# Kernel tuning notes

Hardware: AMD Instinct MI355X
Metric: run time of the kernel (lower is better)

The kernel has to match this reference:

```python
import jax, jax.numpy as jnp
import numpy as np

B, C, E, S, L, N = 2, 256, 256, 3, 5, 128
HMAX = 128
LEVEL_SIZES = np.array([128, 64, 32, 16, 8])
STRIDES = np.array([8.0, 16.0, 32.0, 64.0, 128.0])
GROUPS = 8
EPS = 1e-5


def setup_inputs() -> dict:
    key = jax.random.key(0)
    ks = jax.random.split(key, 16)
    # Padded FPN pyramid stacked as [L, B, C, HMAX, HMAX]; level l valid in [:sz, :sz]
    fm = jnp.zeros((L, B, C, HMAX, HMAX), jnp.float32)
    for l in range(L):
        sz = int(LEVEL_SIZES[l])
        fm = fm.at[l, :, :, :sz, :sz].set(jax.random.normal(ks[l], (B, C, sz, sz), jnp.float32))
    # Boxes in 1024x1024 image coordinates (x1, y1, x2, y2)
    cxy = jax.random.uniform(ks[5], (N, 2), minval=60.0, maxval=960.0)
    wh = jax.random.uniform(ks[6], (N, 2), minval=8.0, maxval=96.0)
    boxes = jnp.concatenate([cxy - wh / 2, cxy + wh / 2], axis=1)
    batch_idx = jax.random.randint(ks[7], (N,), 0, B, jnp.int32)
    level_idx = jax.random.randint(ks[8], (N,), 0, L, jnp.int32)
    sym_ids = jax.random.randint(ks[9], (N,), 0, 6, jnp.int32)
    conv_w = jax.random.normal(ks[10], (E, C, 3, 3), jnp.float32) / np.float32(np.sqrt(C * 9))
    gn_scale = jnp.ones((E,), jnp.float32)
    gn_bias = jnp.zeros((E,), jnp.float32)
    head_w = jax.random.normal(ks[11], (E, E), jnp.float32) / np.float32(np.sqrt(E))
    head_b = jnp.zeros((E,), jnp.float32)
    spat_w = jax.random.normal(ks[12], (E, 4), jnp.float32) * 0.01
    spat_b = jnp.zeros((E,), jnp.float32)
    sym_emb = jax.random.normal(ks[13], (6, E), jnp.float32) * 0.05
    fuse_w = jax.random.normal(ks[14], (6, E, E), jnp.float32) / np.float32(np.sqrt(E))
    fuse_b = jnp.zeros((6, E), jnp.float32)
    return dict(feature_maps=fm, boxes=boxes, conv_w=conv_w, gn_scale=gn_scale,
                gn_bias=gn_bias, head_w=head_w, head_b=head_b, spat_w=spat_w,
                spat_b=spat_b, sym_emb=sym_emb, fuse_w=fuse_w, fuse_b=fuse_b,
                batch_idx=batch_idx, level_idx=level_idx, sym_ids=sym_ids)


def _roi_align(fm, boxes, batch_idx, level_idx):
    # Batched roi_align (aligned=False, sampling_ratio=1) over all boxes at once.
    scale = (1.0 / jnp.asarray(STRIDES, fm.dtype))[level_idx]          # [N]
    hv = jnp.asarray(LEVEL_SIZES, fm.dtype)[level_idx]                 # [N] valid H=W per box
    x1 = boxes[:, 0] * scale; y1 = boxes[:, 1] * scale
    x2 = boxes[:, 2] * scale; y2 = boxes[:, 3] * scale
    roi_w = jnp.maximum(x2 - x1, 1.0)
    roi_h = jnp.maximum(y2 - y1, 1.0)
    off = (jnp.arange(S, dtype=fm.dtype) + 0.5) / S                    # bin centers
    xs = x1[:, None] + off[None, :] * roi_w[:, None]                   # [N,S]
    ys = y1[:, None] + off[None, :] * roi_h[:, None]                   # [N,S]
    y = jnp.broadcast_to(ys[:, :, None], (ys.shape[0], S, S))          # [N,S,S]
    x = jnp.broadcast_to(xs[:, None, :], (xs.shape[0], S, S))
    hvb = hv[:, None, None]
    valid = (y > -1.0) & (y < hvb) & (x > -1.0) & (x < hvb)
    yc = jnp.clip(y, 0.0, hvb - 1.0)
    xc = jnp.clip(x, 0.0, hvb - 1.0)
    y0 = jnp.floor(yc).astype(jnp.int32)
    x0 = jnp.floor(xc).astype(jnp.int32)
    hi = (hvb - 1.0).astype(jnp.int32)
    y1i = jnp.minimum(y0 + 1, hi)
    x1i = jnp.minimum(x0 + 1, hi)
    ly = yc - y0.astype(fm.dtype)
    lx = xc - x0.astype(fm.dtype)
    lvl = level_idx[:, None, None]
    bix = batch_idx[:, None, None]

    def g(yi, xi):
        # gather only the 4 corner pixels -> [N,S,S,C]
        return fm[lvl, bix, :, yi, xi]

    v = ((1 - ly) * (1 - lx))[..., None] * g(y0, x0) \
      + ((1 - ly) * lx)[..., None] * g(y0, x1i) \
      + (ly * (1 - lx))[..., None] * g(y1i, x0) \
      + (ly * lx)[..., None] * g(y1i, x1i)
    v = jnp.where(valid[..., None], v, 0.0)
    return jnp.transpose(v, (0, 3, 1, 2))                              # [N,C,S,S]


def _forward(feature_maps, boxes, conv_w, gn_scale, gn_bias, head_w, head_b,
             spat_w, spat_b, sym_emb, fuse_w, fuse_b, batch_idx, level_idx, sym_ids):
    roi = _roi_align(feature_maps, boxes, batch_idx, level_idx)        # [N,C,S,S]
    h = jax.lax.conv_general_dilated(roi, conv_w, (1, 1), ((1, 1), (1, 1)),
                                     dimension_numbers=('NCHW', 'OIHW', 'NCHW'))  # [N,E,S,S]
    n = h.shape[0]
    hg = h.reshape(n, GROUPS, -1)
    mu = hg.mean(-1, keepdims=True)
    var = hg.var(-1, keepdims=True)
    hg = (hg - mu) * jax.lax.rsqrt(var + EPS)
    h = hg.reshape(h.shape) * gn_scale[None, :, None, None] + gn_bias[None, :, None, None]
    h = jax.nn.relu(h)
    h = h.reshape(n, E, -1).mean(-1)                                   # spatial mean -> [N,E]
    head_out = jax.nn.relu(h @ head_w.T + head_b)                      # sym_feat_nn + ReLU
    spat = jax.nn.relu(boxes @ spat_w.T + spat_b)                      # spatial_embeddings
    fused_in = head_out + spat + sym_emb[sym_ids]                      # + class embedding
    out = jax.nn.relu(jnp.einsum('ne,nfe->nf', fused_in, fuse_w[sym_ids]) + fuse_b[sym_ids])
    return out                                                          # [N,E]


def reference(feature_maps, boxes, conv_w, gn_scale, gn_bias, head_w, head_b,
              spat_w, spat_b, sym_emb, fuse_w, fuse_b, batch_idx, level_idx, sym_ids):
    return _forward(feature_maps, boxes, conv_w, gn_scale, gn_bias, head_w, head_b,
                    spat_w, spat_b, sym_emb, fuse_w, fuse_b, batch_idx, level_idx, sym_ids)
```

## Files before the change

### kernel.cpp

```cpp
#include <hip/hip_runtime.h>
#include <hip/hip_bf16.h>


__device__ __forceinline__ float bf_lo(unsigned u) { return __uint_as_float(u << 16); }
__device__ __forceinline__ float bf_hi(unsigned u) { return __uint_as_float(u & 0xffff0000u); }
__device__ __forceinline__ unsigned short f2bf(float f) {
    __hip_bfloat16 h = __float2bfloat16(f);
    return *(unsigned short*)&h;
}

__global__ __launch_bounds__(256) void prep_k(
    const float* __restrict__ conv_w,
    const float* __restrict__ head_w, const float* __restrict__ fuse_w,
    const float* __restrict__ fm, const float* __restrict__ boxes,
    const int* __restrict__ batch_idx, const int* __restrict__ level_idx,
    unsigned short* __restrict__ w8, unsigned short* __restrict__ w9,
    float* __restrict__ head_wT, float* __restrict__ fuse_wT,
    float* __restrict__ roiT) {
    int blk = blockIdx.x;
    int t = threadIdx.x;

    if (blk < 256) {
        int c = blk, e = t;
        const float* src = conv_w + ((size_t)e * 256 + c) * 9;
        unsigned short tmp[8];
#pragma unroll
        for (int k = 0; k < 8; ++k) tmp[k] = f2bf(src[k]);
        ((uint4*)w8)[(size_t)c * 256 + e] = *(const uint4*)tmp;
        w9[(size_t)c * 256 + e] = f2bf(src[8]);
        return;
    }

    if (blk < 704) {
        __shared__ float tile[32][33];
        int q = blk - 256;
        int z = q >> 6;
        int rem = q & 63;
        int bx = (rem & 7) * 32, by = (rem >> 3) * 32;
        const float* in = (z == 0) ? head_w : fuse_w + (size_t)(z - 1) * 65536;
        float* out = (z == 0) ? head_wT : fuse_wT + (size_t)(z - 1) * 65536;
        int tx = t & 31, ty = t >> 5;
#pragma unroll
        for (int i = 0; i < 32; i += 8)
            tile[ty + i][tx] = in[(size_t)(by + ty + i) * 256 + bx + tx];
        __syncthreads();
#pragma unroll
        for (int i = 0; i < 32; i += 8)
            out[(size_t)(bx + ty + i) * 256 + by + tx] = tile[tx][ty + i];
        return;
    }

    {
        int q = blk - 704;
        int n = q / 9, p = q % 9;
        int i = p / 3, j = p % 3;
        int c = t;

        int lvl = level_idx[n];
        int b = batch_idx[n];
        const float sizes[5]  = {128.f, 64.f, 32.f, 16.f, 8.f};
        const float invstr[5] = {1.f/8.f, 1.f/16.f, 1.f/32.f, 1.f/64.f, 1.f/128.f};
        float scale = invstr[lvl];
        float hv = sizes[lvl];

        float x1 = boxes[n*4+0] * scale, y1 = boxes[n*4+1] * scale;
        float x2 = boxes[n*4+2] * scale, y2 = boxes[n*4+3] * scale;
        float rw = fmaxf(x2 - x1, 1.f), rh = fmaxf(y2 - y1, 1.f);
        float x = x1 + (((float)j + 0.5f) / 3.f) * rw;
        float y = y1 + (((float)i + 0.5f) / 3.f) * rh;

        bool valid = (y > -1.f) && (y < hv) && (x > -1.f) && (x < hv);
        float yc = fminf(fmaxf(y, 0.f), hv - 1.f);
        float xc = fminf(fmaxf(x, 0.f), hv - 1.f);
        int y0 = (int)floorf(yc), x0 = (int)floorf(xc);
        int hi = (int)(hv - 1.f);
        int y1i = min(y0 + 1, hi), x1i = min(x0 + 1, hi);
        float ly = yc - (float)y0, lx = xc - (float)x0;

        const float* base = fm + (((size_t)lvl * 2 + b) * 256 + c) * (128 * 128);
        float v00 = base[y0 * 128 + x0];
        float v01 = base[y0 * 128 + x1i];
        float v10 = base[y1i * 128 + x0];
        float v11 = base[y1i * 128 + x1i];
        float v = (1.f - ly) * (1.f - lx) * v00 + (1.f - ly) * lx * v01 +
                  ly * (1.f - lx) * v10 + ly * lx * v11;
        roiT[((size_t)n * 9 + p) * 256 + c] = valid ? v : 0.f;
    }
}

__global__ __launch_bounds__(512, 2) void conv_gn_pool(
    const float* __restrict__ roiT,
    const unsigned short* __restrict__ w8, const unsigned short* __restrict__ w9,
    const float* __restrict__ gn_scale, const float* __restrict__ gn_bias,
    float* __restrict__ pooled) {
    __shared__ float lds_roi[256 * 12];
    __shared__ float red[4 * 64 * 9];

    int n  = blockIdx.x >> 2;
    int eq = blockIdx.x & 3;
    int t = threadIdx.x;
    int e_loc = t & 63;
    int ch = t >> 6;
    int e = eq * 64 + e_loc;

    const float4* rsrc4 = (const float4*)(roiT + (size_t)n * 2304);
    for (int v4 = t; v4 < 576; v4 += 512) {
        float4 rv = rsrc4[v4];
        int p = v4 / 64, c4 = (v4 & 63) * 4;
        lds_roi[(c4 + 0) * 12 + p] = rv.x;
        lds_roi[(c4 + 1) * 12 + p] = rv.y;
        lds_roi[(c4 + 2) * 12 + p] = rv.z;
        lds_roi[(c4 + 3) * 12 + p] = rv.w;
    }
    __syncthreads();

    float accx[9], accy[9];
#pragma unroll
    for (int p = 0; p < 9; ++p) { accx[p] = 0.f; accy[p] = 0.f; }

    int c0 = ch * 32;
    for (int c = c0; c < c0 + 32; c += 2) {
        float ra[9], rb[9];
#pragma unroll
        for (int jj = 0; jj < 9; ++jj) {
            ra[jj] = lds_roi[c * 12 + jj];
            rb[jj] = lds_roi[(c + 1) * 12 + jj];
        }
        uint4 wa4 = ((const uint4*)w8)[(size_t)c * 256 + e];
        uint4 wb4 = ((const uint4*)w8)[(size_t)(c + 1) * 256 + e];
        float wa[9], wb[9];
        wa[0] = bf_lo(wa4.x); wa[1] = bf_hi(wa4.x);
        wa[2] = bf_lo(wa4.y); wa[3] = bf_hi(wa4.y);
        wa[4] = bf_lo(wa4.z); wa[5] = bf_hi(wa4.z);
        wa[6] = bf_lo(wa4.w); wa[7] = bf_hi(wa4.w);
        wa[8] = bf_lo((unsigned)w9[(size_t)c * 256 + e]);
        wb[0] = bf_lo(wb4.x); wb[1] = bf_hi(wb4.x);
        wb[2] = bf_lo(wb4.y); wb[3] = bf_hi(wb4.y);
        wb[4] = bf_lo(wb4.z); wb[5] = bf_hi(wb4.z);
        wb[6] = bf_lo(wb4.w); wb[7] = bf_hi(wb4.w);
        wb[8] = bf_lo((unsigned)w9[(size_t)(c + 1) * 256 + e]);
#pragma unroll
        for (int ky = 0; ky < 3; ++ky) {
#pragma unroll
            for (int kx = 0; kx < 3; ++kx) {
                float wav = wa[ky * 3 + kx], wbv = wb[ky * 3 + kx];
#pragma unroll
                for (int oy = 0; oy < 3; ++oy) {
                    int iy = oy + ky - 1;
                    if (iy < 0 || iy > 2) continue;
#pragma unroll
                    for (int ox = 0; ox < 3; ++ox) {
                        int ix = ox + kx - 1;
                        if (ix < 0 || ix > 2) continue;
                        int o = oy * 3 + ox, in = iy * 3 + ix;
                        accx[o] = fmaf(wav, ra[in], accx[o]);
                        accy[o] = fmaf(wbv, rb[in], accy[o]);
                    }
                }
            }
        }
    }

    float acc[9];
#pragma unroll
    for (int p = 0; p < 9; ++p) acc[p] = accx[p] + accy[p];

    if (ch >= 4) {
#pragma unroll
        for (int p = 0; p < 9; ++p) red[((ch - 4) * 64 + e_loc) * 9 + p] = acc[p];
    }
    __syncthreads();
    if (ch < 4) {
#pragma unroll
        for (int p = 0; p < 9; ++p) acc[p] += red[(ch * 64 + e_loc) * 9 + p];
    }
    __syncthreads();
    if (ch >= 2 && ch < 4) {
#pragma unroll
        for (int p = 0; p < 9; ++p) red[((ch - 2) * 64 + e_loc) * 9 + p] = acc[p];
    }
    __syncthreads();
    if (ch < 2) {
#pragma unroll
        for (int p = 0; p < 9; ++p) acc[p] += red[(ch * 64 + e_loc) * 9 + p];
    }
    __syncthreads();
    if (ch == 1) {
#pragma unroll
        for (int p = 0; p < 9; ++p) red[e_loc * 9 + p] = acc[p];
    }
    __syncthreads();
    if (ch == 0) {
#pragma unroll
        for (int p = 0; p < 9; ++p) acc[p] += red[e_loc * 9 + p];

        float s = 0.f, sq = 0.f;
#pragma unroll
        for (int p = 0; p < 9; ++p) { s += acc[p]; sq += acc[p] * acc[p]; }
#pragma unroll
        for (int m = 16; m >= 1; m >>= 1) {
            s  += __shfl_xor(s, m, 64);
            sq += __shfl_xor(sq, m, 64);
        }
        float mean = s * (1.f / 288.f);
        float var = sq * (1.f / 288.f) - mean * mean;
        float rinv = rsqrtf(var + 1e-5f);
        float gs = gn_scale[e], gb = gn_bias[e];
        float ps = 0.f;
#pragma unroll
        for (int p = 0; p < 9; ++p) {
            float v = (acc[p] - mean) * rinv * gs + gb;
            ps += fmaxf(v, 0.f);
        }
        pooled[(size_t)n * 256 + e] = ps * (1.f / 9.f);
    }
}

__global__ __launch_bounds__(512) void head_fuse(
    const float* __restrict__ pooled, const float* __restrict__ boxes,
    const float* __restrict__ head_wT, const float* __restrict__ head_b,
    const float* __restrict__ spat_w, const float* __restrict__ spat_b,
    const float* __restrict__ sym_emb,
    const float* __restrict__ fuse_wT, const float* __restrict__ fuse_b,
    const int* __restrict__ sym_ids, float* __restrict__ out) {
    __shared__ float pl[256];
    __shared__ float part[512];
    __shared__ float fin[256];
    int n = blockIdx.x;
    int t = threadIdx.x;
    int e = t & 255;
    int kh = t >> 8;
    int sid = sym_ids[n];

    if (t < 256) pl[t] = pooled[(size_t)n * 256 + t];
    __syncthreads();

    {
        float acc = 0.f;
        const float* w = head_wT + (size_t)(kh * 128) * 256 + e;
        const float* p = pl + kh * 128;
#pragma unroll 8
        for (int k = 0; k < 128; ++k) acc = fmaf(p[k], w[k * 256], acc);
        part[t] = acc;
    }
    __syncthreads();
    if (t < 256) {
        float ho = fmaxf(part[t] + part[t + 256] + head_b[t], 0.f);
        float4 sw = ((const float4*)spat_w)[t];
        float b0 = boxes[n*4+0], b1 = boxes[n*4+1], b2 = boxes[n*4+2], b3 = boxes[n*4+3];
        float sp = fmaxf(spat_b[t] + b0*sw.x + b1*sw.y + b2*sw.z + b3*sw.w, 0.f);
        fin[t] = ho + sp + sym_emb[sid * 256 + t];
    }
    __syncthreads();
    {
        float o = 0.f;
        const float* w = fuse_wT + (size_t)sid * 65536 + (size_t)(kh * 128) * 256 + e;
        const float* p = fin + kh * 128;
#pragma unroll 8
        for (int k = 0; k < 128; ++k) o = fmaf(p[k], w[k * 256], o);
        part[t] = o;
    }
    __syncthreads();
    if (t < 256)
        out[(size_t)n * 256 + t] = fmaxf(part[t] + part[t + 256] + fuse_b[sid * 256 + t], 0.f);
}

extern "C" void kernel_launch(void* const* d_in, const int* in_sizes, int n_in,
                              void* d_out, int out_size, void* d_ws, size_t ws_size,
                              hipStream_t stream) {
    const float* fm      = (const float*)d_in[0];
    const float* boxes   = (const float*)d_in[1];
    const float* conv_w  = (const float*)d_in[2];
    const float* gn_s    = (const float*)d_in[3];
    const float* gn_b    = (const float*)d_in[4];
    const float* head_w  = (const float*)d_in[5];
    const float* head_b  = (const float*)d_in[6];
    const float* spat_w  = (const float*)d_in[7];
    const float* spat_b  = (const float*)d_in[8];
    const float* sym_emb = (const float*)d_in[9];
    const float* fuse_w  = (const float*)d_in[10];
    const float* fuse_b  = (const float*)d_in[11];
    const int* batch_idx = (const int*)d_in[12];
    const int* level_idx = (const int*)d_in[13];
    const int* sym_ids   = (const int*)d_in[14];
    float* outp = (float*)d_out;

    char* ws = (char*)d_ws;
    unsigned short* w8 = (unsigned short*)ws;
    unsigned short* w9 = (unsigned short*)(ws + 1048576);
    float* head_wT = (float*)(ws + 1179648);
    float* fuse_wT = (float*)(ws + 1441792);
    float* roiT    = (float*)(ws + 3014656);
    float* pooled  = (float*)(ws + 4194304);

    prep_k<<<1856, 256, 0, stream>>>(conv_w, head_w, fuse_w, fm, boxes,
                                     batch_idx, level_idx,
                                     w8, w9, head_wT, fuse_wT, roiT);
    conv_gn_pool<<<512, 512, 0, stream>>>(roiT, w8, w9, gn_s, gn_b, pooled);
    head_fuse<<<128, 512, 0, stream>>>(pooled, boxes, head_wT, head_b, spat_w, spat_b,
                                       sym_emb, fuse_wT, fuse_b, sym_ids, outp);
}
```

Measured before the change: 260.1 us.

## Fuse head/fuse MLP into conv kernel via last-block atomic counter epilogue

Removes the separate head_fuse launch by having the last of the four e-quarter blocks for each ROI, detected with a per-ROI atomic counter and threadfences, run the head and fuse matvecs in the conv kernel. The counters are reset in prep_k. This saves one kernel launch and its gap, but adds LDS usage and atomics, and the epilogue runs on only 128 of the blocks, which may leave a serialized tail.

After: 305.1 us. 1.17x slower.

```diff
diff --git a/kernel.cpp b/kernel.cpp
--- a/kernel.cpp
+++ b/kernel.cpp
@@ -16,11 +16,12 @@
     const int* __restrict__ batch_idx, const int* __restrict__ level_idx,
     unsigned short* __restrict__ w8, unsigned short* __restrict__ w9,
     float* __restrict__ head_wT, float* __restrict__ fuse_wT,
-    float* __restrict__ roiT) {
+    float* __restrict__ roiT, int* __restrict__ counter) {
     int blk = blockIdx.x;
     int t = threadIdx.x;
 
     if (blk < 256) {
+        if (blk < 128 && t == 0) counter[blk] = 0;
         int c = blk, e = t;
         const float* src = conv_w + ((size_t)e * 256 + c) * 9;
         unsigned short tmp[8];
@@ -88,13 +89,22 @@
     }
 }
 
-__global__ __launch_bounds__(512, 2) void conv_gn_pool(
+__global__ __launch_bounds__(512, 2) void conv_gn_pool_head(
     const float* __restrict__ roiT,
     const unsigned short* __restrict__ w8, const unsigned short* __restrict__ w9,
     const float* __restrict__ gn_scale, const float* __restrict__ gn_bias,
-    float* __restrict__ pooled) {
+    const float* __restrict__ boxes,
+    const float* __restrict__ head_wT, const float* __restrict__ head_b,
+    const float* __restrict__ spat_w, const float* __restrict__ spat_b,
+    const float* __restrict__ sym_emb,
+    const float* __restrict__ fuse_wT, const float* __restrict__ fuse_b,
+    const int* __restrict__ sym_ids,
+    float* __restrict__ pooled, int* __restrict__ counter,
+    float* __restrict__ out) {
     __shared__ float lds_roi[256 * 12];
     __shared__ float red[4 * 64 * 9];
+    __shared__ float epi[1024];
+    __shared__ int do_epi;
 
     int n  = blockIdx.x >> 2;
     int eq = blockIdx.x & 3;
@@ -214,21 +224,21 @@
         }
         pooled[(size_t)n * 256 + e] = ps * (1.f / 9.f);
     }
-}
-
-__global__ __launch_bounds__(512) void head_fuse(
-    const float* __restrict__ pooled, const float* __restrict__ boxes,
-    const float* __restrict__ head_wT, const float* __restrict__ head_b,
-    const float* __restrict__ spat_w, const float* __restrict__ spat_b,
-    const float* __restrict__ sym_emb,
-    const float* __restrict__ fuse_wT, const float* __restrict__ fuse_b,
-    const int* __restrict__ sym_ids, float* __restrict__ out) {
-    __shared__ float pl[256];
-    __shared__ float part[512];
-    __shared__ float fin[256];
-    int n = blockIdx.x;
-    int t = threadIdx.x;
-    int e = t & 255;
+
+    __syncthreads();
+    if (t == 0) {
+        __threadfence();
+        int old = atomicAdd(&counter[n], 1);
+        do_epi = (old == 3);
+    }
+    __syncthreads();
+    if (!do_epi) return;
+    __threadfence();
+
+    float* pl   = epi;
+    float* part = epi + 256;
+    float* fin  = epi + 768;
+    int e2 = t & 255;
     int kh = t >> 8;
     int sid = sym_ids[n];
 
@@ -236,12 +246,12 @@
     __syncthreads();
 
     {
-        float acc = 0.f;
-        const float* w = head_wT + (size_t)(kh * 128) * 256 + e;
+        float a = 0.f;
+        const float* w = head_wT + (size_t)(kh * 128) * 256 + e2;
         const float* p = pl + kh * 128;
 #pragma unroll 8
-        for (int k = 0; k < 128; ++k) acc = fmaf(p[k], w[k * 256], acc);
-        part[t] = acc;
+        for (int k = 0; k < 128; ++k) a = fmaf(p[k], w[k * 256], a);
+        part[t] = a;
     }
     __syncthreads();
     if (t < 256) {
@@ -254,7 +264,7 @@
     __syncthreads();
     {
         float o = 0.f;
-        const float* w = fuse_wT + (size_t)sid * 65536 + (size_t)(kh * 128) * 256 + e;
+        const float* w = fuse_wT + (size_t)sid * 65536 + (size_t)(kh * 128) * 256 + e2;
         const float* p = fin + kh * 128;
 #pragma unroll 8
         for (int k = 0; k < 128; ++k) o = fmaf(p[k], w[k * 256], o);
@@ -292,11 +302,13 @@
     float* fuse_wT = (float*)(ws + 1441792);
     float* roiT    = (float*)(ws + 3014656);
     float* pooled  = (float*)(ws + 4194304);
+    int*   counter = (int*)(ws + 4325376);
 
     prep_k<<<1856, 256, 0, stream>>>(conv_w, head_w, fuse_w, fm, boxes,
                                      batch_idx, level_idx,
-                                     w8, w9, head_wT, fuse_wT, roiT);
-    conv_gn_pool<<<512, 512, 0, stream>>>(roiT, w8, w9, gn_s, gn_b, pooled);
-    head_fuse<<<128, 512, 0, stream>>>(pooled, boxes, head_wT, head_b, spat_w, spat_b,
-                                       sym_emb, fuse_wT, fuse_b, sym_ids, outp);
+                                     w8, w9, head_wT, fuse_wT, roiT, counter);
+    conv_gn_pool_head<<<512, 512, 0, stream>>>(roiT, w8, w9, gn_s, gn_b,
+                                               boxes, head_wT, head_b, spat_w, spat_b,
+                                               sym_emb, fuse_wT, fuse_b, sym_ids,
+                                               pooled, counter, outp);
 }
```
